# Optimization experiments

Hardware: AMD Instinct MI355X
Metric: run time of the kernel (lower is better)

Reference implementation:

```python
import jax, jax.numpy as jnp
from jax import lax
import numpy as np

NUM_SCALES = 16
MIN_SCALE = 1.0
MAX_SCALE = 16.0
NUM_STEPS = 10
B, C, H, W = 8, 16, 32, 32


def setup_inputs() -> dict:
    key = jax.random.key(0)
    k1, k2, k3 = jax.random.split(key, 3)
    x = jax.random.normal(k1, (B, C, H, W), dtype=jnp.float32)
    scales = jnp.linspace(MIN_SCALE, MAX_SCALE, NUM_SCALES, dtype=jnp.float32)
    f_mod = jax.random.normal(k2, (NUM_STEPS,), dtype=jnp.float32)
    poly_mod = jax.random.normal(k3, (NUM_STEPS, 3), dtype=jnp.float32)
    return {"x": x, "scales": scales, "f_mod": f_mod, "poly_mod": poly_mod, "i": 3}


def _wavelets(scales, f_mod, poly_mod, i, L, dtype):
    # t: [L], f = 1/scale -> sigma = f_mod[i] / (2*pi*f) = f_mod[i]*scale/(2*pi)
    t = jnp.arange(L, dtype=dtype)
    f = 1.0 / scales                                   # [S]
    sigma = f_mod[i] / (2.0 * jnp.pi * f)              # [S]
    u = (t[None, :] / sigma[:, None]) ** 2             # [S, L] = t^2/sigma^2
    poly = 1.0 - poly_mod[i, 0] * u + poly_mod[i, 1] * u**2 + poly_mod[i, 2] * u**3
    return poly * jnp.exp(-0.5 * u)                    # [S, L]


def reference(x, scales, f_mod, poly_mod, i):
    b, c, h, w = x.shape
    L = h * w
    S = scales.shape[0]
    xf = x.reshape(b, c, L)                            # [B, C, L]
    wav = _wavelets(scales, f_mod, poly_mod, i, L, x.dtype)   # [S, L]
    # torch: stack->[S,1,L], .repeat(fdim,1,1) tiles scale-major block C times
    weights = jnp.tile(wav, (c, 1))[:, None, :]        # [C*S, 1, L]
    # torch: x.repeat(1, S, 1) tiles channels S times
    x_rep = jnp.tile(xf, (1, S, 1))                    # [B, C*S, L]
    # torch 'same' padding for even total: extra pad on the right
    pad_l = (L - 1) // 2
    pad_r = (L - 1) - pad_l
    out = lax.conv_general_dilated(
        x_rep, weights,
        window_strides=(1,),
        padding=[(pad_l, pad_r)],
        dimension_numbers=("NCH", "OIH", "NCH"),
        feature_group_count=c * S,
    )                                                   # [B, C*S, L]
    return out
```

## Files before the change

### kernel.cpp

```cpp
#include <hip/hip_runtime.h>
#include <math.h>


__global__ __launch_bounds__(256)
void wavconv_kernel(const float* __restrict__ x,
                    const float* __restrict__ scales,
                    const float* __restrict__ f_mod,
                    const float* __restrict__ poly_mod,
                    const int*   __restrict__ i_ptr,
                    float* __restrict__ out)
{
    __shared__ float xs[1536];
    __shared__ float wv[1024];

    const int tid  = threadIdx.x;
    const int blk  = blockIdx.x;
    const int half = blk & 1;
    const int bc   = blk >> 1;
    const int c    = bc & 15;
    const int b    = bc >> 4;

    const int   ii = i_ptr[0];
    const float fm = f_mod[ii];
    const float p0 = poly_mod[ii * 3 + 0];
    const float p1 = poly_mod[ii * 3 + 1];
    const float p2 = poly_mod[ii * 3 + 2];
    const float sigma = fm * scales[c] * 0.15915494309189535f;
    int kmax = (int)(fabsf(sigma) * 10.0f) + 2;
    if (kmax > 1024) kmax = 1024;

    for (int k = tid; k < kmax; k += 256) {
        const float q  = (float)k / sigma;
        const float u  = q * q;
        const float u2 = u * u;
        const float poly = 1.0f - p0 * u + p1 * u2 + p2 * u2 * u;
        wv[k] = poly * expf(-0.5f * u);
    }

    const int nstage = 512 + kmax;
    const float* __restrict__ xrow = x + ((size_t)bc << 10);
    for (int i = tid; i < nstage; i += 256) {
        const int m = (half << 9) + i - 511;
        xs[i] = (m >= 0 && m < 1024) ? xrow[m] : 0.0f;
    }
    __syncthreads();

    const int lo = tid << 1;
    float a0 = 0.0f, a1 = 0.0f;
    #pragma unroll 4
    for (int k = 0; k < kmax; ++k) {
        const float w = wv[k];
        a0 = fmaf(xs[lo + k],     w, a0);
        a1 = fmaf(xs[lo + 1 + k], w, a1);
    }

    const float2 res = make_float2(a0, a1);
    float* op = out + ((size_t)b << 18) + ((size_t)c << 10) + (half << 9) + lo;
    #pragma unroll
    for (int rep = 0; rep < 16; ++rep) {
        *(float2*)op = res;
        op += 1 << 14;
    }
}

extern "C" void kernel_launch(void* const* d_in, const int* in_sizes, int n_in,
                              void* d_out, int out_size, void* d_ws, size_t ws_size,
                              hipStream_t stream)
{
    const float* x        = (const float*)d_in[0];
    const float* scales   = (const float*)d_in[1];
    const float* f_mod    = (const float*)d_in[2];
    const float* poly_mod = (const float*)d_in[3];
    const int*   i_ptr    = (const int*)d_in[4];
    float* out = (float*)d_out;

    wavconv_kernel<<<256, 256, 0, stream>>>(x, scales, f_mod, poly_mod, i_ptr, out);
}
```

Measured before the change: 10.46 us.

## Skip zero-padded regions per wave and vectorize LDS loads in the convolution loop

For the first half of each row, each wave now starts its convolution at the first tap that touches real data and skips the leading zero padding. Waves whose whole window lies in padding write zeros directly without computing. The inner loop reads four weights as a float4 and the x values as float2 pairs held in rotating registers, which cuts LDS instructions per FMA. It also swaps expf for __expf and division for a reciprocal multiply, and pads the weight buffer with zeros so the 4-wide loop can run past kmax safely.

After: 10.50 us. No clear change (+0.4%).

```diff
diff --git a/kernel.cpp b/kernel.cpp
--- a/kernel.cpp
+++ b/kernel.cpp
@@ -10,8 +10,8 @@
                     const int*   __restrict__ i_ptr,
                     float* __restrict__ out)
 {
-    __shared__ float xs[1536];
-    __shared__ float wv[1024];
+    __shared__ float xs[1552];
+    __shared__ float wv[1032];
 
     const int tid  = threadIdx.x;
     const int blk  = blockIdx.x;
@@ -27,39 +27,61 @@
     const float p2 = poly_mod[ii * 3 + 2];
     const float sigma = fm * scales[c] * 0.15915494309189535f;
     int kmax = (int)(fabsf(sigma) * 10.0f) + 2;
-    if (kmax > 1024) kmax = 1024;
+    if (kmax > 1019) kmax = 1019;
 
-    for (int k = tid; k < kmax; k += 256) {
-        const float q  = (float)k / sigma;
-        const float u  = q * q;
-        const float u2 = u * u;
-        const float poly = 1.0f - p0 * u + p1 * u2 + p2 * u2 * u;
-        wv[k] = poly * expf(-0.5f * u);
-    }
-
-    const int nstage = 512 + kmax;
+    const int nstage = kmax + 520;
     const float* __restrict__ xrow = x + ((size_t)bc << 10);
     for (int i = tid; i < nstage; i += 256) {
         const int m = (half << 9) + i - 511;
         xs[i] = (m >= 0 && m < 1024) ? xrow[m] : 0.0f;
     }
+
+    const float rs = 1.0f / sigma;
+    for (int k = tid; k < kmax + 4; k += 256) {
+        const float q  = (float)k * rs;
+        const float u  = q * q;
+        const float u2 = u * u;
+        const float poly = 1.0f - p0 * u + p1 * u2 + p2 * u2 * u;
+        const float val  = poly * __expf(-0.5f * u);
+        wv[k] = (k < kmax) ? val : 0.0f;
+    }
+
+    const int lo  = tid << 1;
+    const int wlo = (tid >> 6) << 7;
+    int kst = 0;
+    if (half == 0) { kst = 384 - wlo; if (kst < 0) kst = 0; }
+    const bool zwave = (half == 0) && (384 - wlo >= kmax);
+
+    float* op = out + ((size_t)b << 18) + ((size_t)c << 10) + (half << 9) + lo;
+
+    if (zwave) {
+        const float2 z = make_float2(0.0f, 0.0f);
+        float* p = op;
+        #pragma unroll
+        for (int rep = 0; rep < 16; ++rep) { *(float2*)p = z; p += 1 << 14; }
+    }
+
     __syncthreads();
 
-    const int lo = tid << 1;
-    float a0 = 0.0f, a1 = 0.0f;
-    #pragma unroll 4
-    for (int k = 0; k < kmax; ++k) {
-        const float w = wv[k];
-        a0 = fmaf(xs[lo + k],     w, a0);
-        a1 = fmaf(xs[lo + 1 + k], w, a1);
-    }
-
-    const float2 res = make_float2(a0, a1);
-    float* op = out + ((size_t)b << 18) + ((size_t)c << 10) + (half << 9) + lo;
-    #pragma unroll
-    for (int rep = 0; rep < 16; ++rep) {
-        *(float2*)op = res;
-        op += 1 << 14;
+    if (!zwave) {
+        float a0 = 0.0f, a1 = 0.0f;
+        float2 A = *(const float2*)&xs[lo + kst];
+        float2 B = *(const float2*)&xs[lo + kst + 2];
+        #pragma unroll 4
+        for (int k = kst; k < kmax; k += 4) {
+            const float4 w4 = *(const float4*)&wv[k];
+            const float2 C  = *(const float2*)&xs[lo + k + 4];
+            const float2 D  = *(const float2*)&xs[lo + k + 6];
+            a0 = fmaf(A.x, w4.x, a0); a0 = fmaf(A.y, w4.y, a0);
+            a0 = fmaf(B.x, w4.z, a0); a0 = fmaf(B.y, w4.w, a0);
+            a1 = fmaf(A.y, w4.x, a1); a1 = fmaf(B.x, w4.y, a1);
+            a1 = fmaf(B.y, w4.z, a1); a1 = fmaf(C.x, w4.w, a1);
+            A = C; B = D;
+        }
+        const float2 res = make_float2(a0, a1);
+        float* p = op;
+        #pragma unroll
+        for (int rep = 0; rep < 16; ++rep) { *(float2*)p = res; p += 1 << 14; }
     }
 }
 
```
